# Kernel optimization log

Measured on AMD Instinct MI355X. Metric: run time of the kernel, lower is better.

The kernel has to match this reference:

```python
import jax, jax.numpy as jnp
import numpy as np

N, M = 4096, 8192
NFEAT, EFEAT, NHID, NCLASS = 128, 64, 64, 16
ALPHA = 0.2
NEG = -9e15
BN_SCALE = np.float32(1.0 / np.sqrt(1.0 + 1e-5))  # eval BatchNorm: running stats (0,1), affine (1,0)


def _masked_att(hs, hd, a, mask):
    # hs: [P,F], hd: [Q,F], a: [2F], mask: [P,Q] binary
    F_ = hs.shape[1]
    logits = (hs @ a[:F_])[:, None] + (hd @ a[F_:])[None, :]            # [P,Q]
    logits = jnp.where(mask > 0, jax.nn.leaky_relu(logits, ALPHA), NEG)
    return jax.nn.softmax(logits, axis=1) @ hd                           # [P,F]


def _gat_layer(x, ex, adj, eadj, nem, Wn, We, ann, ane, aee, aen, concat):
    h = x @ Wn                                  # [N,F]
    g = ex @ We                                 # [M,F]
    Hn = _masked_att(h, h, ann, adj)            # node <- node neighbors
    He = _masked_att(h, g, ane, nem)            # node <- incident edges
    Ge = _masked_att(g, g, aee, eadj)           # edge <- adjacent edges
    Gn = _masked_att(g, h, aen, nem.T)          # edge <- endpoint nodes
    if concat:
        return (jax.nn.elu(jnp.concatenate([Hn, He], axis=1)),
                jax.nn.elu(jnp.concatenate([Ge, Gn], axis=1)))
    return Hn + He, Ge + Gn


def _mlp(h, W1, b1, W2, b2):
    h = jax.nn.relu((h @ W1 + b1) * BN_SCALE)
    return h @ W2 + b2


def _next_layer(h, A, W1, b1, W2, b2):
    pooled = A @ h                              # spmm(adj, h), dense-stored
    rep = _mlp(pooled, W1, b1, W2, b2)
    return jax.nn.relu(rep * BN_SCALE)


def setup_inputs() -> dict:
    key = jax.random.key(0)
    ks = jax.random.split(key, 40)
    f32 = jnp.float32
    x = jax.random.normal(ks[0], (N, NFEAT), f32)
    e_x = jax.random.normal(ks[1], (M, EFEAT), f32)
    adj = jnp.minimum((jax.random.uniform(ks[2], (N, N)) < 16.0 / N).astype(f32) + jnp.eye(N, dtype=f32), 1.0)
    e_adj = jnp.minimum((jax.random.uniform(ks[3], (M, M)) < 16.0 / M).astype(f32) + jnp.eye(M, dtype=f32), 1.0)
    n_e_adj = (jax.random.uniform(ks[4], (N, M)) < 4.0 / M).astype(f32)

    def lin(k, i, o):
        return jax.random.normal(k, (i, o), f32) * np.float32(1.0 / np.sqrt(i))

    def avec(k, F_):
        return jax.random.normal(k, (2 * F_,), f32) * np.float32(0.1)

    d = dict(x=x, e_x=e_x, adj=adj, e_adj=e_adj, n_e_adj=n_e_adj)
    # layer dims: (node_in, edge_in, out)
    dims = [(NFEAT, EFEAT, NHID), (2 * NHID, 2 * NHID, 2 * NHID), (64, 64, NCLASS)]
    ki = 5
    for li, (ni, ei, fo) in enumerate(dims):
        d[f'l{li}_Wn'] = lin(ks[ki], ni, fo); ki += 1
        d[f'l{li}_We'] = lin(ks[ki], ei, fo); ki += 1
        for nm in ('ann', 'ane', 'aee', 'aen'):
            d[f'l{li}_{nm}'] = avec(ks[ki], fo); ki += 1
    mdims = [(256, 64, 64), (64, 64, 64)]
    for mi, (i_, h_, o_) in enumerate(mdims):
        d[f'm{mi}_W1'] = lin(ks[ki], i_, h_); ki += 1
        d[f'm{mi}_b1'] = jnp.zeros((h_,), f32)
        d[f'm{mi}_W2'] = lin(ks[ki], h_, o_); ki += 1
        d[f'm{mi}_b2'] = jnp.zeros((o_,), f32)
    return d


def reference(x, e_x, adj, e_adj, n_e_adj,
              l0_Wn, l0_We, l0_ann, l0_ane, l0_aee, l0_aen,
              l1_Wn, l1_We, l1_ann, l1_ane, l1_aee, l1_aen,
              l2_Wn, l2_We, l2_ann, l2_ane, l2_aee, l2_aen,
              m0_W1, m0_b1, m0_W2, m0_b2,
              m1_W1, m1_b1, m1_W2, m1_b2):
    # dropout is identity in eval mode
    h, g = _gat_layer(x, e_x, adj, e_adj, n_e_adj, l0_Wn, l0_We, l0_ann, l0_ane, l0_aee, l0_aen, True)
    h, g = _gat_layer(h, g, adj, e_adj, n_e_adj, l1_Wn, l1_We, l1_ann, l1_ane, l1_aee, l1_aen, True)
    h_n, h_e = h, g
    h_n = _next_layer(h_n, adj, m0_W1, m0_b1, m0_W2, m0_b2)
    h_n = _next_layer(h_n, adj, m1_W1, m1_b1, m1_W2, m1_b2)
    h_e = _next_layer(h_e, e_adj, m0_W1, m0_b1, m0_W2, m0_b2)
    h_e = _next_layer(h_e, e_adj, m1_W1, m1_b1, m1_W2, m1_b2)
    fn, fe = _gat_layer(h_n, h_e, adj, e_adj, n_e_adj, l2_Wn, l2_We, l2_ann, l2_ane, l2_aee, l2_aen, False)
    return (jax.nn.log_softmax(jax.nn.elu(fn), axis=1),
            jax.nn.log_softmax(jax.nn.elu(fe), axis=1))
```

## Files before the change

### kernel.cpp

```cpp
#include <hip/hip_runtime.h>
#include <cmath>

constexpr int N_ = 4096;
constexpr int M_ = 8192;
constexpr float ALPHA_ = 0.2f;
constexpr float BN_SC = 0.9999950000374998f;
constexpr int CAP = 64;

typedef unsigned long long u64;

__device__ __forceinline__ float lrelu(float x) { return x > 0.f ? x : ALPHA_ * x; }
__device__ __forceinline__ float elu(float x) { return x > 0.f ? x : __expf(x) - 1.f; }

__global__ __launch_bounds__(256) void csr_build(
    const float* __restrict__ adj, const float* __restrict__ eadj, const float* __restrict__ nem,
    int* __restrict__ cA, int* __restrict__ iA,
    int* __restrict__ cE, int* __restrict__ iE,
    int* __restrict__ cN, int* __restrict__ iN,
    int* __restrict__ cT, int* __restrict__ iT) {
  int wid = blockIdx.x * 4 + (threadIdx.x >> 6);
  int lane = threadIdx.x & 63;
  const float* mask; int row, Q; int* cnt; int* idx; bool tr = false;
  if (wid < N_)           { mask = adj;  row = wid;            Q = N_; cnt = cA; idx = iA; }
  else if (wid < N_ + M_) { mask = eadj; row = wid - N_;       Q = M_; cnt = cE; idx = iE; }
  else                    { mask = nem;  row = wid - N_ - M_;  Q = M_; cnt = cN; idx = iN; tr = true; }
  const float* mr = mask + (size_t)row * Q;
  u64 lt = (1ull << lane) - 1ull;
  int total = 0;
  for (int q0 = 0; q0 < Q; q0 += 256) {
    float4 v = *reinterpret_cast<const float4*>(mr + q0 + lane * 4);
    unsigned mk = (v.x > 0.5f ? 1u : 0u) | (v.y > 0.5f ? 2u : 0u) |
                  (v.z > 0.5f ? 4u : 0u) | (v.w > 0.5f ? 8u : 0u);
    u64 b0 = __ballot(mk & 1u), b1 = __ballot(mk & 2u), b2 = __ballot(mk & 4u), b3 = __ballot(mk & 8u);
    if (mk) {
      int base = total + __popcll(b0 & lt) + __popcll(b1 & lt) + __popcll(b2 & lt) + __popcll(b3 & lt);
      int ob = 0;
#pragma unroll
      for (int e = 0; e < 4; e++) {
        if (mk & (1u << e)) {
          int pos = base + ob;
          int j = q0 + lane * 4 + e;
          if (pos < CAP) idx[(size_t)row * CAP + pos] = j;
          if (tr) {
            int tp = atomicAdd(&cT[j], 1);
            if (tp < CAP) iT[(size_t)j * CAP + tp] = row;
          }
          ob++;
        }
      }
    }
    total += __popcll(b0) + __popcll(b1) + __popcll(b2) + __popcll(b3);
  }
  if (lane == 0) cnt[row] = min(total, CAP);
}

__global__ __launch_bounds__(256) void sortT(int* __restrict__ cT, int* __restrict__ iT) {
  int j = blockIdx.x * 4 + (threadIdx.x >> 6);
  int lane = threadIdx.x & 63;
  if (j >= M_) return;
  int n = min(cT[j], CAP);
  int v = lane < n ? iT[(size_t)j * CAP + lane] : 0x7fffffff;
#pragma unroll
  for (int k = 2; k <= 64; k <<= 1) {
#pragma unroll
    for (int s = k >> 1; s > 0; s >>= 1) {
      int o = __shfl_xor(v, s);
      bool up = ((lane & k) == 0);
      bool keepmin = (((lane & s) == 0) == up);
      v = keepmin ? min(v, o) : max(v, o);
    }
  }
  if (lane < n) iT[(size_t)j * CAP + lane] = v;
  if (lane == 0) cT[j] = n;
}

struct PDOp {
  const float* X; const float* W; int K, P;
  const float* a0; const float* a1; const float* a2; const float* a3;
  float* o0; float* o1; float* o2; float* o3;
  float* Y;
};

template <int F>
__global__ __launch_bounds__(512) void projdots(PDOp A, PDOp B) {
  PDOp op = blockIdx.y == 0 ? A : B;
  constexpr int RPB = 512 / F;
  constexpr int KC = 8192 / F;
  __shared__ float Wl[8192];
  __shared__ float dred[8][4];
  int rl = threadIdx.x / F;
  int f = threadIdx.x % F;
  int p = blockIdx.x * RPB + rl;
  bool act = p < op.P;
  float acc = 0.f;
  for (int k0 = 0; k0 < op.K; k0 += KC) {
    int kc = min(KC, op.K - k0);
    __syncthreads();
    for (int i = threadIdx.x; i < kc * F; i += 512) Wl[i] = op.W[(size_t)k0 * F + i];
    __syncthreads();
    if (act) {
      const float4* xr4 = reinterpret_cast<const float4*>(op.X + (size_t)p * op.K + k0);
      for (int k = 0; k < kc; k += 4) {
        float4 xv = xr4[k >> 2];
        acc = fmaf(xv.x, Wl[k * F + f], acc);
        acc = fmaf(xv.y, Wl[(k + 1) * F + f], acc);
        acc = fmaf(xv.z, Wl[(k + 2) * F + f], acc);
        acc = fmaf(xv.w, Wl[(k + 3) * F + f], acc);
      }
    }
  }
  if (act) op.Y[(size_t)p * F + f] = acc;
  float q0 = acc * op.a0[f];
  float q1 = acc * op.a1[f];
  float q2 = acc * op.a2[f];
  float q3 = acc * op.a3[f];
  constexpr int WID = F < 64 ? F : 64;
#pragma unroll
  for (int t = 1; t < WID; t <<= 1) {
    q0 += __shfl_xor(q0, t, WID);
    q1 += __shfl_xor(q1, t, WID);
    q2 += __shfl_xor(q2, t, WID);
    q3 += __shfl_xor(q3, t, WID);
  }
  if constexpr (F == 128) {
    int w = threadIdx.x >> 6;
    if ((threadIdx.x & 63) == 0) { dred[w][0] = q0; dred[w][1] = q1; dred[w][2] = q2; dred[w][3] = q3; }
    __syncthreads();
    if (act && f == 0) {
      int w0 = rl * 2;
      op.o0[p] = dred[w0][0] + dred[w0 + 1][0];
      op.o1[p] = dred[w0][1] + dred[w0 + 1][1];
      op.o2[p] = dred[w0][2] + dred[w0 + 1][2];
      op.o3[p] = dred[w0][3] + dred[w0 + 1][3];
    }
  } else {
    if (act && f == 0) { op.o0[p] = q0; op.o1[p] = q1; op.o2[p] = q2; op.o3[p] = q3; }
  }
}

struct COp { const float* X; int Q, F; };

__global__ __launch_bounds__(256) void colsum_p(COp A, COp B, float* __restrict__ part) {
  COp op = blockIdx.y == 0 ? A : B;
  int f = threadIdx.x;
  float acc = 0.f;
  if (f < op.F) {
    int per = op.Q / 128;
    int j0 = blockIdx.x * per;
    for (int j = j0; j < j0 + per; j++) acc += op.X[(size_t)j * op.F + f];
  }
  if (f < 128) part[((size_t)blockIdx.y * 128 + blockIdx.x) * 128 + f] = acc;
}

__global__ __launch_bounds__(256) void colsum_r(const float* __restrict__ part, int Fh, int Fg,
                                                float* __restrict__ oh, float* __restrict__ og) {
  int y = blockIdx.y;
  int f = threadIdx.x;
  int F = y ? Fg : Fh;
  float* o = y ? og : oh;
  if (f >= F) return;
  float s = 0.f;
  for (int b = 0; b < 128; b++) s += part[((size_t)y * 128 + b) * 128 + f];
  o[f] = s;
}

struct AOp {
  const int* cnt; const int* idx; const float* s; const float* d;
  const float* Hd; const float* cs; float* out; int ldo, ocol, P, Q;
};

template <int F>
__global__ __launch_bounds__(256) void att4(AOp A0, AOp A1, AOp A2, AOp A3) {
  int y = blockIdx.y;
  AOp op = y == 0 ? A0 : y == 1 ? A1 : y == 2 ? A2 : A3;
  constexpr int C = F / 64;
  int row = blockIdx.x * 4 + (threadIdx.x >> 6);
  int lane = threadIdx.x & 63;
  if (row >= op.P) return;
  int n = op.cnt[row];
  float acc[C];
  if (n == 0) {
    float invQ = 1.f / (float)op.Q;
#pragma unroll
    for (int c = 0; c < C; c++) acc[c] = op.cs[lane + c * 64] * invQ;
  } else {
    float sp = op.s[row];
    const int* ip = op.idx + (size_t)row * CAP;
    int jl = lane < n ? ip[lane] : 0;
    float dl = lane < n ? op.d[jl] : -INFINITY;
    float mm = dl;
#pragma unroll
    for (int t = 1; t < 64; t <<= 1) mm = fmaxf(mm, __shfl_xor(mm, t));
    float m = lrelu(sp + mm);
    float el = lane < n ? __expf(lrelu(sp + dl) - m) : 0.f;
    float l = el;
#pragma unroll
    for (int t = 1; t < 64; t <<= 1) l += __shfl_xor(l, t);
    float invl = 1.f / l;
#pragma unroll
    for (int c = 0; c < C; c++) acc[c] = 0.f;
    int k = 0;
    for (; k + 2 <= n; k += 2) {
      int j0 = __shfl(jl, k), j1 = __shfl(jl, k + 1);
      float e0 = __shfl(el, k), e1 = __shfl(el, k + 1);
      const float* h0 = op.Hd + (size_t)j0 * F + lane;
      const float* h1 = op.Hd + (size_t)j1 * F + lane;
#pragma unroll
      for (int c = 0; c < C; c++) acc[c] = fmaf(e0, h0[c * 64], fmaf(e1, h1[c * 64], acc[c]));
    }
    if (k < n) {
      int j0 = __shfl(jl, k);
      float e0 = __shfl(el, k);
#pragma unroll
      for (int c = 0; c < C; c++) acc[c] = fmaf(e0, op.Hd[(size_t)j0 * F + lane + c * 64], acc[c]);
    }
#pragma unroll
    for (int c = 0; c < C; c++) acc[c] *= invl;
  }
  float* o = op.out + (size_t)row * op.ldo + op.ocol + lane;
#pragma unroll
  for (int c = 0; c < C; c++) o[c * 64] = elu(acc[c]);
}

template <int C>
__global__ __launch_bounds__(256) void nextlayer(
    const int* __restrict__ cA, const int* __restrict__ iA,
    const int* __restrict__ cE, const int* __restrict__ iE,
    const float* __restrict__ HdN, const float* __restrict__ HdM,
    const float* __restrict__ W1, const float* __restrict__ b1,
    const float* __restrict__ W2, const float* __restrict__ b2,
    float* __restrict__ outN, float* __restrict__ outM) {
  constexpr int KD = C * 64;
  int y = blockIdx.y;
  const int* cnt = y ? cE : cA;
  const int* idx = y ? iE : iA;
  const float* Hd = y ? HdM : HdN;
  float* out = y ? outM : outN;
  int P = y ? M_ : N_;
  int w = threadIdx.x >> 6, lane = threadIdx.x & 63;
  int row = blockIdx.x * 4 + w;
  if (row >= P) return;
  int n = cnt[row];
  const int* ip = idx + (size_t)row * CAP;
  int jl = lane < n ? ip[lane] : 0;
  float acc[C];
#pragma unroll
  for (int c = 0; c < C; c++) acc[c] = 0.f;
  int k = 0;
  for (; k + 2 <= n; k += 2) {
    int j0 = __shfl(jl, k), j1 = __shfl(jl, k + 1);
    const float* h0 = Hd + (size_t)j0 * KD + lane;
    const float* h1 = Hd + (size_t)j1 * KD + lane;
#pragma unroll
    for (int c = 0; c < C; c++) acc[c] += h0[c * 64] + h1[c * 64];
  }
  if (k < n) {
    int j0 = __shfl(jl, k);
#pragma unroll
    for (int c = 0; c < C; c++) acc[c] += Hd[(size_t)j0 * KD + lane + c * 64];
  }
  float y1 = 0.f;
#pragma unroll
  for (int c = 0; c < C; c++) {
    for (int kk = 0; kk < 64; kk++)
      y1 = fmaf(__shfl(acc[c], kk), W1[(c * 64 + kk) * 64 + lane], y1);
  }
  y1 = fmaxf((y1 + b1[lane]) * BN_SC, 0.f);
  float y2 = 0.f;
  for (int kk = 0; kk < 64; kk++)
    y2 = fmaf(__shfl(y1, kk), W2[kk * 64 + lane], y2);
  out[(size_t)row * 64 + lane] = fmaxf((y2 + b2[lane]) * BN_SC, 0.f);
}

__device__ __forceinline__ float att_col16(const int* cnt, const int* idx, float sp,
                                           const float* d, const float* Hd,
                                           const float* cs, int Q, int row, int c) {
  int n = cnt[row];
  if (n == 0) return cs[c] / (float)Q;
  const int* ip = idx + (size_t)row * CAP;
  float mm = -INFINITY;
  for (int k0 = 0; k0 < n; k0 += 16) {
    int k = k0 + c;
    float dv = k < n ? d[ip[k]] : -INFINITY;
    mm = fmaxf(mm, dv);
  }
#pragma unroll
  for (int t = 1; t < 16; t <<= 1) mm = fmaxf(mm, __shfl_xor(mm, t, 16));
  float m = lrelu(sp + mm);
  float l = 0.f, a = 0.f;
  for (int k0 = 0; k0 < n; k0 += 16) {
    int k = k0 + c;
    int jx = k < n ? ip[k] : 0;
    float dv = k < n ? d[jx] : 0.f;
    float ex = k < n ? __expf(lrelu(sp + dv) - m) : 0.f;
    int kmax = min(16, n - k0);
    for (int kk = 0; kk < kmax; kk++) {
      float e = __shfl(ex, kk, 16);
      int j = __shfl(jx, kk, 16);
      l += e;
      a = fmaf(e, Hd[(size_t)j * 16 + c], a);
    }
  }
  return a / l;
}

__global__ __launch_bounds__(256) void att_final(
    const int* __restrict__ cA, const int* __restrict__ iA, const float* __restrict__ s0, const float* __restrict__ d0,
    const int* __restrict__ cN, const int* __restrict__ iN, const float* __restrict__ s1, const float* __restrict__ d1,
    const int* __restrict__ cE, const int* __restrict__ iE, const float* __restrict__ s2, const float* __restrict__ d2,
    const int* __restrict__ cT, const int* __restrict__ iT, const float* __restrict__ s3, const float* __restrict__ d3,
    const float* __restrict__ h2, const float* __restrict__ g2,
    const float* __restrict__ csh, const float* __restrict__ csg,
    float* __restrict__ out) {
  int y = blockIdx.y;
  int gid = blockIdx.x * 256 + threadIdx.x;
  int row = gid >> 4, c = gid & 15;
  float v; float* dst;
  if (y == 0) {
    if (row >= N_) return;
    v = att_col16(cA, iA, s0[row], d0, h2, csh, N_, row, c)
      + att_col16(cN, iN, s1[row], d1, g2, csg, M_, row, c);
    dst = out + (size_t)row * 16 + c;
  } else {
    if (row >= M_) return;
    v = att_col16(cE, iE, s2[row], d2, g2, csg, M_, row, c)
      + att_col16(cT, iT, s3[row], d3, h2, csh, N_, row, c);
    dst = out + (size_t)(N_ + row) * 16 + c;
  }
  v = elu(v);
  float mx = v;
#pragma unroll
  for (int t = 1; t < 16; t <<= 1) mx = fmaxf(mx, __shfl_xor(mx, t, 16));
  float ex = __expf(v - mx);
  float sm = ex;
#pragma unroll
  for (int t = 1; t < 16; t <<= 1) sm += __shfl_xor(sm, t, 16);
  *dst = v - mx - __logf(sm);
}

extern "C" void kernel_launch(void* const* d_in, const int* in_sizes, int n_in,
                              void* d_out, int out_size, void* d_ws, size_t ws_size,
                              hipStream_t stream) {
  (void)in_sizes; (void)n_in; (void)out_size; (void)ws_size;
  const float* x    = (const float*)d_in[0];
  const float* e_x  = (const float*)d_in[1];
  const float* adj  = (const float*)d_in[2];
  const float* eadj = (const float*)d_in[3];
  const float* nem  = (const float*)d_in[4];
  const float* l_Wn[3]  = {(const float*)d_in[5],  (const float*)d_in[11], (const float*)d_in[17]};
  const float* l_We[3]  = {(const float*)d_in[6],  (const float*)d_in[12], (const float*)d_in[18]};
  const float* l_ann[3] = {(const float*)d_in[7],  (const float*)d_in[13], (const float*)d_in[19]};
  const float* l_ane[3] = {(const float*)d_in[8],  (const float*)d_in[14], (const float*)d_in[20]};
  const float* l_aee[3] = {(const float*)d_in[9],  (const float*)d_in[15], (const float*)d_in[21]};
  const float* l_aen[3] = {(const float*)d_in[10], (const float*)d_in[16], (const float*)d_in[22]};
  const float* m_W1[2] = {(const float*)d_in[23], (const float*)d_in[27]};
  const float* m_b1[2] = {(const float*)d_in[24], (const float*)d_in[28]};
  const float* m_W2[2] = {(const float*)d_in[25], (const float*)d_in[29]};
  const float* m_b2[2] = {(const float*)d_in[26], (const float*)d_in[30]};
  float* outp = (float*)d_out;

  char* wsp = (char*)d_ws;
  size_t off = 0;
  auto alloc = [&](size_t bytes) -> void* {
    void* p = wsp + off;
    off += (bytes + 255) & ~(size_t)255;
    return p;
  };
  int* cT = (int*)alloc((size_t)M_ * 4);
  size_t zero_bytes = off;

  float* csg = (float*)alloc(3 * 128 * 4);
  float* csh = (float*)alloc(3 * 128 * 4);
  float* cspart = (float*)alloc((size_t)2 * 128 * 128 * 4);

  int* cA = (int*)alloc((size_t)N_ * 4);
  int* cE = (int*)alloc((size_t)M_ * 4);
  int* cN = (int*)alloc((size_t)N_ * 4);
  int* iA = (int*)alloc((size_t)N_ * CAP * 4);
  int* iE = (int*)alloc((size_t)M_ * CAP * 4);
  int* iN = (int*)alloc((size_t)N_ * CAP * 4);
  int* iT = (int*)alloc((size_t)M_ * CAP * 4);

  float* ht  = (float*)alloc((size_t)N_ * 128 * 4);
  float* gt  = (float*)alloc((size_t)M_ * 128 * 4);
  float* hA  = (float*)alloc((size_t)N_ * 128 * 4);
  float* gA  = (float*)alloc((size_t)M_ * 128 * 4);
  float* hB  = (float*)alloc((size_t)N_ * 256 * 4);
  float* gB  = (float*)alloc((size_t)M_ * 256 * 4);
  float* h64a = (float*)alloc((size_t)N_ * 64 * 4);
  float* g64a = (float*)alloc((size_t)M_ * 64 * 4);
  float* h64b = (float*)alloc((size_t)N_ * 64 * 4);
  float* g64b = (float*)alloc((size_t)M_ * 64 * 4);
  float* h16 = (float*)alloc((size_t)N_ * 16 * 4);
  float* g16 = (float*)alloc((size_t)M_ * 16 * 4);
  float* s0N = (float*)alloc((size_t)N_ * 4);
  float* d0N = (float*)alloc((size_t)N_ * 4);
  float* s1N = (float*)alloc((size_t)N_ * 4);
  float* d3N = (float*)alloc((size_t)N_ * 4);
  float* d1M = (float*)alloc((size_t)M_ * 4);
  float* s2M = (float*)alloc((size_t)M_ * 4);
  float* d2M = (float*)alloc((size_t)M_ * 4);
  float* s3M = (float*)alloc((size_t)M_ * 4);

  dim3 B(256);
  hipMemsetAsync(wsp, 0, zero_bytes, stream);

  csr_build<<<dim3((2 * N_ + M_) / 4), B, 0, stream>>>(adj, eadj, nem, cA, iA, cE, iE, cN, iN, cT, iT);
  sortT<<<dim3(M_ / 4), B, 0, stream>>>(cT, iT);

  auto runPD = [&](int F, const float* Xh, int Kh, const float* Xg, int Kg, float* Yh, float* Yg, int li) {
    PDOp Ah{Xh, l_Wn[li], Kh, N_, l_ann[li], l_ann[li] + F, l_ane[li], l_aen[li] + F,
            s0N, d0N, s1N, d3N, Yh};
    PDOp Bg{Xg, l_We[li], Kg, M_, l_ane[li] + F, l_aee[li], l_aee[li] + F, l_aen[li],
            d1M, s2M, d2M, s3M, Yg};
    int rpb = 512 / F;
    if (F == 64)       projdots<64><<<dim3(M_ / rpb, 2), dim3(512), 0, stream>>>(Ah, Bg);
    else if (F == 128) projdots<128><<<dim3(M_ / rpb, 2), dim3(512), 0, stream>>>(Ah, Bg);
    else               projdots<16><<<dim3(M_ / rpb, 2), dim3(512), 0, stream>>>(Ah, Bg);
  };
  auto runCs = [&](const float* h, const float* g, int F, int li) {
    colsum_p<<<dim3(128, 2), B, 0, stream>>>(COp{h, N_, F}, COp{g, M_, F}, cspart);
    colsum_r<<<dim3(1, 2), B, 0, stream>>>(cspart, F, F, csh + li * 128, csg + li * 128);
  };

  runPD(64, x, 128, e_x, 64, ht, gt, 0);
  runCs(ht, gt, 64, 0);
  att4<64><<<dim3(M_ / 4, 4), B, 0, stream>>>(
      AOp{cA, iA, s0N, d0N, ht, csh + 0, hA, 128, 0, N_, N_},
      AOp{cN, iN, s1N, d1M, gt, csg + 0, hA, 128, 64, N_, M_},
      AOp{cE, iE, s2M, d2M, gt, csg + 0, gA, 128, 0, M_, M_},
      AOp{cT, iT, s3M, d3N, ht, csh + 0, gA, 128, 64, M_, N_});

  runPD(128, hA, 128, gA, 128, ht, gt, 1);
  runCs(ht, gt, 128, 1);
  att4<128><<<dim3(M_ / 4, 4), B, 0, stream>>>(
      AOp{cA, iA, s0N, d0N, ht, csh + 128, hB, 256, 0, N_, N_},
      AOp{cN, iN, s1N, d1M, gt, csg + 128, hB, 256, 128, N_, M_},
      AOp{cE, iE, s2M, d2M, gt, csg + 128, gB, 256, 0, M_, M_},
      AOp{cT, iT, s3M, d3N, ht, csh + 128, gB, 256, 128, M_, N_});

  nextlayer<4><<<dim3(M_ / 4, 2), B, 0, stream>>>(cA, iA, cE, iE, hB, gB,
                                                  m_W1[0], m_b1[0], m_W2[0], m_b2[0], h64a, g64a);
  nextlayer<1><<<dim3(M_ / 4, 2), B, 0, stream>>>(cA, iA, cE, iE, h64a, g64a,
                                                  m_W1[1], m_b1[1], m_W2[1], m_b2[1], h64b, g64b);

  runPD(16, h64b, 64, g64b, 64, h16, g16, 2);
  runCs(h16, g16, 16, 2);
  att_final<<<dim3(M_ * 16 / 256, 2), B, 0, stream>>>(
      cA, iA, s0N, d0N, cN, iN, s1N, d1M, cE, iE, s2M, d2M, cT, iT, s3M, d3N,
      h16, g16, csh + 256, csg + 256, outp);
}
```

Measured before the change: 365.7 us.

## Fuse CSR build with first projection and fold colsum and sort into consumers

Runs CSR construction and the layer-0 projection in one launch as separate grid slices. The transpose sort moves into the first attention kernel, which sorts each row's indices in place on first use. The separate column-sum kernels are replaced by per-block partial sums written in the projection epilogue, which attention rows with no neighbours reduce themselves. This removes several small launches and serial dependencies, but every empty row now walks up to 2048 partial vectors, which can be expensive because many transpose rows are empty.

```diff
diff --git a/kernel.cpp b/kernel.cpp
--- a/kernel.cpp
+++ b/kernel.cpp
@@ -12,18 +12,18 @@
 __device__ __forceinline__ float lrelu(float x) { return x > 0.f ? x : ALPHA_ * x; }
 __device__ __forceinline__ float elu(float x) { return x > 0.f ? x : __expf(x) - 1.f; }
 
-__global__ __launch_bounds__(256) void csr_build(
-    const float* __restrict__ adj, const float* __restrict__ eadj, const float* __restrict__ nem,
-    int* __restrict__ cA, int* __restrict__ iA,
-    int* __restrict__ cE, int* __restrict__ iE,
-    int* __restrict__ cN, int* __restrict__ iN,
-    int* __restrict__ cT, int* __restrict__ iT) {
-  int wid = blockIdx.x * 4 + (threadIdx.x >> 6);
+struct CsrA {
+  const float* adj; const float* eadj; const float* nem;
+  int* cA; int* iA; int* cE; int* iE; int* cN; int* iN; int* cT; int* iT;
+};
+
+__device__ void csr_body(const CsrA& a) {
+  int wid = blockIdx.x * 8 + (threadIdx.x >> 6);
   int lane = threadIdx.x & 63;
   const float* mask; int row, Q; int* cnt; int* idx; bool tr = false;
-  if (wid < N_)           { mask = adj;  row = wid;            Q = N_; cnt = cA; idx = iA; }
-  else if (wid < N_ + M_) { mask = eadj; row = wid - N_;       Q = M_; cnt = cE; idx = iE; }
-  else                    { mask = nem;  row = wid - N_ - M_;  Q = M_; cnt = cN; idx = iN; tr = true; }
+  if (wid < N_)           { mask = a.adj;  row = wid;            Q = N_; cnt = a.cA; idx = a.iA; }
+  else if (wid < N_ + M_) { mask = a.eadj; row = wid - N_;       Q = M_; cnt = a.cE; idx = a.iE; }
+  else                    { mask = a.nem;  row = wid - N_ - M_;  Q = M_; cnt = a.cN; idx = a.iN; tr = true; }
   const float* mr = mask + (size_t)row * Q;
   u64 lt = (1ull << lane) - 1ull;
   int total = 0;
@@ -42,8 +42,8 @@
           int j = q0 + lane * 4 + e;
           if (pos < CAP) idx[(size_t)row * CAP + pos] = j;
           if (tr) {
-            int tp = atomicAdd(&cT[j], 1);
-            if (tp < CAP) iT[(size_t)j * CAP + tp] = row;
+            int tp = atomicAdd(&a.cT[j], 1);
+            if (tp < CAP) a.iT[(size_t)j * CAP + tp] = row;
           }
           ob++;
         }
@@ -52,26 +52,6 @@
     total += __popcll(b0) + __popcll(b1) + __popcll(b2) + __popcll(b3);
   }
   if (lane == 0) cnt[row] = min(total, CAP);
-}
-
-__global__ __launch_bounds__(256) void sortT(int* __restrict__ cT, int* __restrict__ iT) {
-  int j = blockIdx.x * 4 + (threadIdx.x >> 6);
-  int lane = threadIdx.x & 63;
-  if (j >= M_) return;
-  int n = min(cT[j], CAP);
-  int v = lane < n ? iT[(size_t)j * CAP + lane] : 0x7fffffff;
-#pragma unroll
-  for (int k = 2; k <= 64; k <<= 1) {
-#pragma unroll
-    for (int s = k >> 1; s > 0; s >>= 1) {
-      int o = __shfl_xor(v, s);
-      bool up = ((lane & k) == 0);
-      bool keepmin = (((lane & s) == 0) == up);
-      v = keepmin ? min(v, o) : max(v, o);
-    }
-  }
-  if (lane < n) iT[(size_t)j * CAP + lane] = v;
-  if (lane == 0) cT[j] = n;
 }
 
 struct PDOp {
@@ -82,8 +62,7 @@
 };
 
 template <int F>
-__global__ __launch_bounds__(512) void projdots(PDOp A, PDOp B) {
-  PDOp op = blockIdx.y == 0 ? A : B;
+__device__ void proj_body(const PDOp& op, float* part) {
   constexpr int RPB = 512 / F;
   constexpr int KC = 8192 / F;
   __shared__ float Wl[8192];
@@ -136,37 +115,35 @@
   } else {
     if (act && f == 0) { op.o0[p] = q0; op.o1[p] = q1; op.o2[p] = q2; op.o3[p] = q3; }
   }
-}
-
-struct COp { const float* X; int Q, F; };
-
-__global__ __launch_bounds__(256) void colsum_p(COp A, COp B, float* __restrict__ part) {
-  COp op = blockIdx.y == 0 ? A : B;
-  int f = threadIdx.x;
-  float acc = 0.f;
-  if (f < op.F) {
-    int per = op.Q / 128;
-    int j0 = blockIdx.x * per;
-    for (int j = j0; j < j0 + per; j++) acc += op.X[(size_t)j * op.F + f];
-  }
-  if (f < 128) part[((size_t)blockIdx.y * 128 + blockIdx.x) * 128 + f] = acc;
-}
-
-__global__ __launch_bounds__(256) void colsum_r(const float* __restrict__ part, int Fh, int Fg,
-                                                float* __restrict__ oh, float* __restrict__ og) {
-  int y = blockIdx.y;
-  int f = threadIdx.x;
-  int F = y ? Fg : Fh;
-  float* o = y ? og : oh;
-  if (f >= F) return;
-  float s = 0.f;
-  for (int b = 0; b < 128; b++) s += part[((size_t)y * 128 + b) * 128 + f];
-  o[f] = s;
+  float* sred = Wl;
+  __syncthreads();
+  sred[rl * F + f] = act ? acc : 0.f;
+  __syncthreads();
+  if (rl == 0) {
+    float s = 0.f;
+    for (int r = 0; r < RPB; r++) s += sred[r * F + f];
+    part[(size_t)blockIdx.x * F + f] = s;
+  }
+}
+
+__global__ __launch_bounds__(512) void phase0(CsrA ca, PDOp A, PDOp B,
+                                              float* partH, float* partG) {
+  if (blockIdx.y == 0) { csr_body(ca); return; }
+  if (blockIdx.x >= M_ / 8) return;
+  if (blockIdx.y == 1) proj_body<64>(A, partH);
+  else                 proj_body<64>(B, partG);
+}
+
+template <int F>
+__global__ __launch_bounds__(512) void proj_l(PDOp A, PDOp B, float* partH, float* partG) {
+  if (blockIdx.y == 0) proj_body<F>(A, partH);
+  else                 proj_body<F>(B, partG);
 }
 
 struct AOp {
-  const int* cnt; const int* idx; const float* s; const float* d;
-  const float* Hd; const float* cs; float* out; int ldo, ocol, P, Q;
+  const int* cnt; int* idx; const float* s; const float* d;
+  const float* Hd; const float* part; int nb; float* out; int ldo, ocol, P, Q;
+  int sortL; int* cTw;
 };
 
 template <int F>
@@ -177,16 +154,39 @@
   int row = blockIdx.x * 4 + (threadIdx.x >> 6);
   int lane = threadIdx.x & 63;
   if (row >= op.P) return;
-  int n = op.cnt[row];
+  int n = min(op.cnt[row], CAP);
   float acc[C];
   if (n == 0) {
+#pragma unroll
+    for (int c = 0; c < C; c++) acc[c] = 0.f;
+    for (int b = 0; b < op.nb; b++) {
+#pragma unroll
+      for (int c = 0; c < C; c++) acc[c] += op.part[(size_t)b * F + lane + c * 64];
+    }
     float invQ = 1.f / (float)op.Q;
 #pragma unroll
-    for (int c = 0; c < C; c++) acc[c] = op.cs[lane + c * 64] * invQ;
+    for (int c = 0; c < C; c++) acc[c] *= invQ;
   } else {
     float sp = op.s[row];
-    const int* ip = op.idx + (size_t)row * CAP;
-    int jl = lane < n ? ip[lane] : 0;
+    int* ip = op.idx + (size_t)row * CAP;
+    int jl;
+    if (op.sortL) {
+      int v = lane < n ? ip[lane] : 0x7fffffff;
+#pragma unroll
+      for (int k = 2; k <= 64; k <<= 1) {
+#pragma unroll
+        for (int s = k >> 1; s > 0; s >>= 1) {
+          int o = __shfl_xor(v, s);
+          bool keepmin = (((lane & s) == 0) == ((lane & k) == 0));
+          v = keepmin ? min(v, o) : max(v, o);
+        }
+      }
+      if (lane < n) ip[lane] = v;
+      if (lane == 0) op.cTw[row] = n;
+      jl = v;
+    } else {
+      jl = lane < n ? ip[lane] : 0;
+    }
     float dl = lane < n ? op.d[jl] : -INFINITY;
     float mm = dl;
 #pragma unroll
@@ -240,7 +240,7 @@
   int w = threadIdx.x >> 6, lane = threadIdx.x & 63;
   int row = blockIdx.x * 4 + w;
   if (row >= P) return;
-  int n = cnt[row];
+  int n = min(cnt[row], CAP);
   const int* ip = idx + (size_t)row * CAP;
   int jl = lane < n ? ip[lane] : 0;
   float acc[C];
@@ -274,9 +274,13 @@
 
 __device__ __forceinline__ float att_col16(const int* cnt, const int* idx, float sp,
                                            const float* d, const float* Hd,
-                                           const float* cs, int Q, int row, int c) {
-  int n = cnt[row];
-  if (n == 0) return cs[c] / (float)Q;
+                                           const float* part, int nb, int Q, int row, int c) {
+  int n = min(cnt[row], CAP);
+  if (n == 0) {
+    float s = 0.f;
+    for (int b = 0; b < nb; b++) s += part[b * 16 + c];
+    return s / (float)Q;
+  }
   const int* ip = idx + (size_t)row * CAP;
   float mm = -INFINITY;
   for (int k0 = 0; k0 < n; k0 += 16) {
@@ -310,7 +314,7 @@
     const int* __restrict__ cE, const int* __restrict__ iE, const float* __restrict__ s2, const float* __restrict__ d2,
     const int* __restrict__ cT, const int* __restrict__ iT, const float* __restrict__ s3, const float* __restrict__ d3,
     const float* __restrict__ h2, const float* __restrict__ g2,
-    const float* __restrict__ csh, const float* __restrict__ csg,
+    const float* __restrict__ partH, const float* __restrict__ partG, int nb,
     float* __restrict__ out) {
   int y = blockIdx.y;
   int gid = blockIdx.x * 256 + threadIdx.x;
@@ -318,13 +322,13 @@
   float v; float* dst;
   if (y == 0) {
     if (row >= N_) return;
-    v = att_col16(cA, iA, s0[row], d0, h2, csh, N_, row, c)
-      + att_col16(cN, iN, s1[row], d1, g2, csg, M_, row, c);
+    v = att_col16(cA, iA, s0[row], d0, h2, partH, nb, N_, row, c)
+      + att_col16(cN, iN, s1[row], d1, g2, partG, nb, M_, row, c);
     dst = out + (size_t)row * 16 + c;
   } else {
     if (row >= M_) return;
-    v = att_col16(cE, iE, s2[row], d2, g2, csg, M_, row, c)
-      + att_col16(cT, iT, s3[row], d3, h2, csh, N_, row, c);
+    v = att_col16(cE, iE, s2[row], d2, g2, partG, nb, M_, row, c)
+      + att_col16(cT, iT, s3[row], d3, h2, partH, nb, N_, row, c);
     dst = out + (size_t)(N_ + row) * 16 + c;
   }
   v = elu(v);
@@ -369,9 +373,8 @@
   int* cT = (int*)alloc((size_t)M_ * 4);
   size_t zero_bytes = off;
 
-  float* csg = (float*)alloc(3 * 128 * 4);
-  float* csh = (float*)alloc(3 * 128 * 4);
-  float* cspart = (float*)alloc((size_t)2 * 128 * 128 * 4);
+  float* bufH = (float*)alloc((size_t)2048 * 128 * 4);
+  float* bufG = (float*)alloc((size_t)2048 * 128 * 4);
 
   int* cA = (int*)alloc((size_t)N_ * 4);
   int* cE = (int*)alloc((size_t)M_ * 4);
@@ -402,51 +405,48 @@
   float* d2M = (float*)alloc((size_t)M_ * 4);
   float* s3M = (float*)alloc((size_t)M_ * 4);
 
-  dim3 B(256);
   hipMemsetAsync(wsp, 0, zero_bytes, stream);
 
-  csr_build<<<dim3((2 * N_ + M_) / 4), B, 0, stream>>>(adj, eadj, nem, cA, iA, cE, iE, cN, iN, cT, iT);
-  sortT<<<dim3(M_ / 4), B, 0, stream>>>(cT, iT);
-
-  auto runPD = [&](int F, const float* Xh, int Kh, const float* Xg, int Kg, float* Yh, float* Yg, int li) {
+  auto mkA = [&](int F, const float* Xh, int Kh, const float* Xg, int Kg, float* Yh, float* Yg, int li) {
     PDOp Ah{Xh, l_Wn[li], Kh, N_, l_ann[li], l_ann[li] + F, l_ane[li], l_aen[li] + F,
             s0N, d0N, s1N, d3N, Yh};
     PDOp Bg{Xg, l_We[li], Kg, M_, l_ane[li] + F, l_aee[li], l_aee[li] + F, l_aen[li],
             d1M, s2M, d2M, s3M, Yg};
-    int rpb = 512 / F;
-    if (F == 64)       projdots<64><<<dim3(M_ / rpb, 2), dim3(512), 0, stream>>>(Ah, Bg);
-    else if (F == 128) projdots<128><<<dim3(M_ / rpb, 2), dim3(512), 0, stream>>>(Ah, Bg);
-    else               projdots<16><<<dim3(M_ / rpb, 2), dim3(512), 0, stream>>>(Ah, Bg);
+    return std::make_pair(Ah, Bg);
   };
-  auto runCs = [&](const float* h, const float* g, int F, int li) {
-    colsum_p<<<dim3(128, 2), B, 0, stream>>>(COp{h, N_, F}, COp{g, M_, F}, cspart);
-    colsum_r<<<dim3(1, 2), B, 0, stream>>>(cspart, F, F, csh + li * 128, csg + li * 128);
-  };
-
-  runPD(64, x, 128, e_x, 64, ht, gt, 0);
-  runCs(ht, gt, 64, 0);
-  att4<64><<<dim3(M_ / 4, 4), B, 0, stream>>>(
-      AOp{cA, iA, s0N, d0N, ht, csh + 0, hA, 128, 0, N_, N_},
-      AOp{cN, iN, s1N, d1M, gt, csg + 0, hA, 128, 64, N_, M_},
-      AOp{cE, iE, s2M, d2M, gt, csg + 0, gA, 128, 0, M_, M_},
-      AOp{cT, iT, s3M, d3N, ht, csh + 0, gA, 128, 64, M_, N_});
-
-  runPD(128, hA, 128, gA, 128, ht, gt, 1);
-  runCs(ht, gt, 128, 1);
-  att4<128><<<dim3(M_ / 4, 4), B, 0, stream>>>(
-      AOp{cA, iA, s0N, d0N, ht, csh + 128, hB, 256, 0, N_, N_},
-      AOp{cN, iN, s1N, d1M, gt, csg + 128, hB, 256, 128, N_, M_},
-      AOp{cE, iE, s2M, d2M, gt, csg + 128, gB, 256, 0, M_, M_},
-      AOp{cT, iT, s3M, d3N, ht, csh + 128, gB, 256, 128, M_, N_});
-
-  nextlayer<4><<<dim3(M_ / 4, 2), B, 0, stream>>>(cA, iA, cE, iE, hB, gB,
-                                                  m_W1[0], m_b1[0], m_W2[0], m_b2[0], h64a, g64a);
-  nextlayer<1><<<dim3(M_ / 4, 2), B, 0, stream>>>(cA, iA, cE, iE, h64a, g64a,
-                                                  m_W1[1], m_b1[1], m_W2[1], m_b2[1], h64b, g64b);
-
-  runPD(16, h64b, 64, g64b, 64, h16, g16, 2);
-  runCs(h16, g16, 16, 2);
-  att_final<<<dim3(M_ * 16 / 256, 2), B, 0, stream>>>(
+
+  {
+    CsrA ca{adj, eadj, nem, cA, iA, cE, iE, cN, iN, cT, iT};
+    auto ab = mkA(64, x, 128, e_x, 64, ht, gt, 0);
+    phase0<<<dim3(2048, 3), dim3(512), 0, stream>>>(ca, ab.first, ab.second, bufH, bufG);
+  }
+
+  att4<64><<<dim3(M_ / 4, 4), dim3(256), 0, stream>>>(
+      AOp{cA, iA, s0N, d0N, ht, bufH, 1024, hA, 128, 0, N_, N_, 0, nullptr},
+      AOp{cN, iN, s1N, d1M, gt, bufG, 1024, hA, 128, 64, N_, M_, 0, nullptr},
+      AOp{cE, iE, s2M, d2M, gt, bufG, 1024, gA, 128, 0, M_, M_, 0, nullptr},
+      AOp{cT, iT, s3M, d3N, ht, bufH, 1024, gA, 128, 64, M_, N_, 1, cT});
+
+  {
+    auto ab = mkA(128, hA, 128, gA, 128, ht, gt, 1);
+    proj_l<128><<<dim3(2048, 2), dim3(512), 0, stream>>>(ab.first, ab.second, bufH, bufG);
+  }
+  att4<128><<<dim3(M_ / 4, 4), dim3(256), 0, stream>>>(
+      AOp{cA, iA, s0N, d0N, ht, bufH, 2048, hB, 256, 0, N_, N_, 0, nullptr},
+      AOp{cN, iN, s1N, d1M, gt, bufG, 2048, hB, 256, 128, N_, M_, 0, nullptr},
+      AOp{cE, iE, s2M, d2M, gt, bufG, 2048, gB, 256, 0, M_, M_, 0, nullptr},
+      AOp{cT, iT, s3M, d3N, ht, bufH, 2048, gB, 256, 128, M_, N_, 0, nullptr});
+
+  nextlayer<4><<<dim3(M_ / 4, 2), dim3(256), 0, stream>>>(cA, iA, cE, iE, hB, gB,
+      m_W1[0], m_b1[0], m_W2[0], m_b2[0], h64a, g64a);
+  nextlayer<1><<<dim3(M_ / 4, 2), dim3(256), 0, stream>>>(cA, iA, cE, iE, h64a, g64a,
+      m_W1[1], m_b1[1], m_W2[1], m_b2[1], h64b, g64b);
+
+  {
+    auto ab = mkA(16, h64b, 64, g64b, 64, h16, g16, 2);
+    proj_l<16><<<dim3(256, 2), dim3(512), 0, stream>>>(ab.first, ab.second, bufH, bufG);
+  }
+  att_final<<<dim3(M_ * 16 / 256, 2), dim3(256), 0, stream>>>(
       cA, iA, s0N, d0N, cN, iN, s1N, d1M, cE, iE, s2M, d2M, cT, iT, s3M, d3N,
-      h16, g16, csh + 256, csg + 256, outp);
-}
+      h16, g16, bufH, bufG, 256, outp);
+}
```

New measurement: 1.059 ms. 190% more time.
